# Optimization experiments

Measured on AMD Instinct MI355X. Metric: run time of the kernel, lower is better.

## Reference

```python
import jax, jax.numpy as jnp
import numpy as np

B, H, W = 2, 64, 1024
C1, C2 = 64, 128
MLP = [128, 128]
KH, KW = 5, 5
NS = 3
DIST = 100.0
BN_EPS = 1e-5


def setup_inputs() -> dict:
    key = jax.random.key(0)
    ks = jax.random.split(key, 12)
    inp = {
        "xyz1_proj": jax.random.normal(ks[0], (B, H, W, 3), jnp.float32),
        "xyz2_proj": jax.random.normal(ks[1], (B, H, W, 3), jnp.float32),
        "feat1_proj": jax.random.normal(ks[2], (B, H, W, C1), jnp.float32),
        "feat2_proj": jax.random.normal(ks[3], (B, H, W, C2), jnp.float32),
    }
    cin = C1 + C2
    chans = [cin] + MLP
    for i in range(len(MLP)):
        inp[f"w{i}"] = jax.random.normal(ks[4 + 2 * i], (chans[i], chans[i + 1]), jnp.float32) * 0.05
        inp[f"b{i}"] = jnp.zeros((chans[i + 1],), jnp.float32)
        inp[f"g{i}"] = jnp.ones((chans[i + 1],), jnp.float32)
        inp[f"be{i}"] = jnp.zeros((chans[i + 1],), jnp.float32)
    return inp


def _grid_knn(xyz1, xyz2):
    """Structured-grid KNN (no_sort_knn): for each query pixel, scan a KHxKW
    window in row-major order and take the first NS in-bounds neighbors whose
    squared distance is below DIST^2. Returns flat neighbor indices (B,N,NS)
    and a validity mask (B,N,NS,1)."""
    b, h, w, _ = xyz1.shape
    n = h * w
    k = KH * KW
    x1 = xyz1.reshape(b, n, 3)
    x2 = xyz2.reshape(b, n, 3)
    oh = jnp.repeat(jnp.arange(KH) - KH // 2, KW)   # (K,)
    ow = jnp.tile(jnp.arange(KW) - KW // 2, KH)     # (K,)
    nh = jnp.arange(h)[:, None, None] + oh[None, None, :]   # (H,1,K)
    nw = jnp.arange(w)[None, :, None] + ow[None, None, :]   # (1,W,K)
    inb = ((nh >= 0) & (nh < h)) & ((nw >= 0) & (nw < w))    # (H,W,K)
    flat = jnp.clip(nh, 0, h - 1) * w + jnp.clip(nw, 0, w - 1)
    flat = jnp.broadcast_to(flat, (h, w, k)).reshape(n, k)
    inb = jnp.broadcast_to(inb, (h, w, k)).reshape(n, k)
    # window gather: (B,N,K,3)
    neigh = jnp.take(x2, flat.reshape(-1), axis=1).reshape(b, n, k, 3)
    sq = jnp.sum(jnp.square(neigh - x1[:, :, None, :]), -1)  # (B,N,K)
    valid = inb[None] & (sq < DIST * DIST)
    v = valid.astype(jnp.int32)
    rank = jnp.cumsum(v, -1) - v  # rank among valid, scan order
    sel, fnd = [], []
    for j in range(NS):
        hit = valid & (rank == j)
        sel.append(jnp.argmax(hit, -1))
        fnd.append(jnp.any(hit, -1))
    sel = jnp.stack(sel, -1)          # (B,N,NS) window slot
    found = jnp.stack(fnd, -1)        # (B,N,NS)
    flat_b = jnp.broadcast_to(flat[None], (b, n, k))
    sel_flat = jnp.take_along_axis(flat_b, sel, axis=-1)
    sel_flat = jnp.where(found, sel_flat, 0)  # zeros like the init buffers
    mask = found.astype(x1.dtype)[..., None]  # (B,N,NS,1)
    return sel_flat, mask


def _gather(feat_flat, sel_flat):
    # feat_flat: (B,N,C), sel_flat: (B,N,NS) -> (B,N,NS,C)
    b, n, c = feat_flat.shape
    idx = sel_flat.reshape(b, n * NS, 1)
    g = jnp.take_along_axis(feat_flat, jnp.broadcast_to(idx, (b, n * NS, c)), axis=1)
    return g.reshape(b, n, NS, c)


def reference(xyz1_proj, xyz2_proj, feat1_proj, feat2_proj,
              w0, b0, g0, be0, w1, b1, g1, be1):
    b, h, w, _ = xyz1_proj.shape
    n = h * w
    xyz1 = xyz1_proj.reshape(b, n, 3)
    xyz2 = xyz2_proj.reshape(b, n, 3)
    feat2 = feat2_proj.reshape(b, n, -1)

    sel_flat, mask = _grid_knn(xyz1_proj, xyz2_proj)
    mask = jax.lax.stop_gradient(mask)

    grouped_xyz = _gather(xyz2, sel_flat) * mask          # (B,N,NS,3)
    grouped_feat = _gather(feat2, sel_flat) * mask        # (B,N,NS,C2)

    dist = jnp.sum(jnp.square(grouped_xyz - xyz1[:, :, None, :]), -1)  # (B,N,NS)
    dist = jnp.where(dist < 1e-10, jnp.full_like(dist, 1e-10), dist)
    norm = jnp.sum(1.0 / dist, axis=2, keepdims=True)     # (B,N,1)
    weight = (1.0 / dist) / norm                          # (B,N,NS)
    interp = jnp.sum(grouped_feat * weight[..., None], axis=2)  # (B,N,C2)

    x = jnp.concatenate([feat1_proj.reshape(b, n, -1), interp], -1)  # (B,N,C1+C2)

    # 1x1 conv MLP with training-mode BatchNorm + ReLU
    for (wi, bi, gi, bei) in ((w0, b0, g0, be0), (w1, b1, g1, be1)):
        x = x @ wi + bi
        mu = jnp.mean(x, axis=(0, 1))
        var = jnp.var(x, axis=(0, 1))
        x = (x - mu) * jax.lax.rsqrt(var + BN_EPS) * gi + bei
        x = jax.nn.relu(x)
    return x  # (B, H*W, MLP[-1])
```

## Files before the change

kernel.cpp:

```cpp
#include <hip/hip_runtime.h>

#define H_    64
#define W_    1024
#define NPT   65536
#define NTOT  131072
#define C1_   64
#define C2_   128
#define CIN_  192
#define CM_   128
#define NS_   3
#define DIST2_ 10000.0f
#define BN_EPS_ 1e-5f
#define NSLOT 32
#define XP    132

typedef __attribute__((ext_vector_type(8))) short short8;
typedef __attribute__((ext_vector_type(4))) float floatx4;

static __device__ __forceinline__ unsigned short f2bf(float f) {
    unsigned int u = __float_as_uint(f);
    u += 0x7fffu + ((u >> 16) & 1u);
    return (unsigned short)(u >> 16);
}
static __device__ __forceinline__ float bflo(unsigned u) { return __uint_as_float(u << 16); }
static __device__ __forceinline__ float bfhi(unsigned u) { return __uint_as_float(u & 0xffff0000u); }
static __device__ __forceinline__ unsigned packbf(float a, float b) {
    return (unsigned)f2bf(a) | ((unsigned)f2bf(b) << 16);
}

__global__ __launch_bounds__(256) void prep_w_kernel(
    const float* __restrict__ w0, const float* __restrict__ w1,
    unsigned short* __restrict__ w0F, unsigned short* __restrict__ w1F)
{
    int tid = blockIdx.x * 256 + threadIdx.x;
    if (tid < 3072) {
        int c = tid, lane = c & 63, nt = (c >> 6) & 7, kk = c >> 9;
        int n = nt * 16 + (lane & 15);
        int kb = kk * 32 + (lane >> 4) * 8;
        #pragma unroll
        for (int j = 0; j < 8; j++)
            w0F[(size_t)c * 8 + j] = f2bf(w0[(size_t)(kb + j) * CM_ + n]);
    } else if (tid < 5120) {
        int c = tid - 3072, lane = c & 63, nt = (c >> 6) & 7, kk = c >> 9;
        int n = nt * 16 + (lane & 15);
        int kb = kk * 32 + (lane >> 4) * 8;
        #pragma unroll
        for (int j = 0; j < 8; j++)
            w1F[(size_t)c * 8 + j] = f2bf(w1[(size_t)(kb + j) * CM_ + n]);
    }
}

static __device__ __forceinline__ void bn_finish_lds(
    const float* __restrict__ slots, const float* __restrict__ g,
    const float* __restrict__ be, float* bnpL, int t)
{
    if (t < CM_) {
        float s = 0.f, q2 = 0.f;
        #pragma unroll
        for (int sl = 0; sl < NSLOT; sl++) {
            s  += slots[sl * 256 + t];
            q2 += slots[sl * 256 + CM_ + t];
        }
        const float invn = 1.0f / (float)NTOT;
        float mu = s * invn, var = q2 * invn - mu * mu;
        float sc = g[t] * rsqrtf(var + BN_EPS_);
        bnpL[t] = sc;
        bnpL[CM_ + t] = be[t] - mu * sc;
    }
}

__global__ __launch_bounds__(256, 2) void fused1_kernel(
    const float* __restrict__ xyz1, const float* __restrict__ xyz2,
    const float* __restrict__ feat1, const float* __restrict__ feat2,
    const unsigned short* __restrict__ w0F, const float* __restrict__ b0,
    uint4* __restrict__ y0w4, float* __restrict__ slots0)
{
    __shared__ unsigned short xstage[64][XP];
    __shared__ int   selL[64][NS_];
    __shared__ float wgtL[64][NS_];
    __shared__ float wsum[4][CM_], wsq[4][CM_];

    const int t = threadIdx.x;
    const int blk = blockIdx.x;
    const int pbase = blk * 64;
    const int bidx = blk >> 10;
    const int wv = t >> 6, lane = t & 63;
    const int m = lane & 15, q = lane >> 4;
    const int lr = wv * 16 + m;
    const int row0 = pbase + lr;

    short8 af[2];
    #pragma unroll
    for (int kk = 0; kk < 2; kk++) {
        const float* sp = feat1 + (size_t)row0 * C1_ + kk * 32 + q * 8;
        float4 fa = *(const float4*)(sp), fb = *(const float4*)(sp + 4);
        short8 a;
        a[0] = f2bf(fa.x); a[1] = f2bf(fa.y); a[2] = f2bf(fa.z); a[3] = f2bf(fa.w);
        a[4] = f2bf(fb.x); a[5] = f2bf(fb.y); a[6] = f2bf(fb.z); a[7] = f2bf(fb.w);
        af[kk] = a;
    }

    if (t < 64) {
        const int pt = pbase + t;
        const int n = pt & (NPT - 1);
        const int h = n >> 10, w = n & (W_ - 1);
        const float* p1 = xyz1 + (size_t)pt * 3;
        float x1 = p1[0], y1 = p1[1], z1 = p1[2];
        const float* x2b = xyz2 + (size_t)bidx * NPT * 3;

        float sq[25];
        #pragma unroll
        for (int k = 0; k < 25; k++) {
            const int dh = k / 5 - 2, dw = k % 5 - 2;
            int nh = h + dh, nw = w + dw;
            bool inb = (nh >= 0) && (nh < H_) && (nw >= 0) && (nw < W_);
            int ch = min(max(nh, 0), H_ - 1);
            int cw = min(max(nw, 0), W_ - 1);
            const float* p2 = x2b + (size_t)(ch * W_ + cw) * 3;
            float dx = p2[0] - x1, dy = p2[1] - y1, dz = p2[2] - z1;
            float s = dx * dx + dy * dy + dz * dz;
            sq[k] = inb ? s : 3.4e38f;
        }
        int   s0 = 0, s1 = 0, s2 = 0;
        float d0 = 0.f, d1 = 0.f, d2 = 0.f;
        int cnt = 0;
        #pragma unroll
        for (int k = 0; k < 25; k++) {
            const int dh = k / 5 - 2, dw = k % 5 - 2;
            int ch = min(max(h + dh, 0), H_ - 1);
            int cw = min(max(w + dw, 0), W_ - 1);
            int nidx = ch * W_ + cw;
            if (sq[k] < DIST2_ && cnt < NS_) {
                if (cnt == 0)      { s0 = nidx; d0 = sq[k]; }
                else if (cnt == 1) { s1 = nidx; d1 = sq[k]; }
                else               { s2 = nidx; d2 = sq[k]; }
                cnt++;
            }
        }
        float self2 = x1 * x1 + y1 * y1 + z1 * z1;
        float dd0 = (cnt > 0) ? d0 : self2;
        float dd1 = (cnt > 1) ? d1 : self2;
        float dd2 = (cnt > 2) ? d2 : self2;
        dd0 = fmaxf(dd0, 1e-10f); dd1 = fmaxf(dd1, 1e-10f); dd2 = fmaxf(dd2, 1e-10f);
        float i0 = 1.0f / dd0, i1 = 1.0f / dd1, i2 = 1.0f / dd2;
        float norm = i0 + i1 + i2;
        selL[t][0] = (cnt > 0) ? s0 : 0;
        selL[t][1] = (cnt > 1) ? s1 : 0;
        selL[t][2] = (cnt > 2) ? s2 : 0;
        wgtL[t][0] = (cnt > 0) ? i0 / norm : 0.f;
        wgtL[t][1] = (cnt > 1) ? i1 / norm : 0.f;
        wgtL[t][2] = (cnt > 2) ? i2 / norm : 0.f;
    }
    __syncthreads();

    const float* f2b = feat2 + (size_t)bidx * NPT * C2_;
    #pragma unroll
    for (int i = 0; i < 8; i++) {
        int idx = t + i * 256;
        int p = idx >> 5, c4 = (idx & 31) << 2;
        float ax = 0.f, ay = 0.f, az = 0.f, aw = 0.f;
        #pragma unroll
        for (int j = 0; j < NS_; j++) {
            float wj = wgtL[p][j];
            const float4 f = *(const float4*)(f2b + (size_t)selL[p][j] * C2_ + c4);
            ax += wj * f.x; ay += wj * f.y; az += wj * f.z; aw += wj * f.w;
        }
        ushort4 u;
        u.x = f2bf(ax); u.y = f2bf(ay); u.z = f2bf(az); u.w = f2bf(aw);
        *(ushort4*)&xstage[p][c4] = u;
    }
    __syncthreads();

    floatx4 acc[8];
    #pragma unroll
    for (int nt = 0; nt < 8; nt++) acc[nt] = (floatx4){0.f, 0.f, 0.f, 0.f};

    #pragma unroll
    for (int kk = 0; kk < 6; kk++) {
        short8 bw[8];
        #pragma unroll
        for (int nt = 0; nt < 8; nt++)
            bw[nt] = *(const short8*)(w0F + ((size_t)(kk * 8 + nt) * 64 + lane) * 8);
        short8 a = (kk < 2) ? af[kk]
                            : *(const short8*)&xstage[lr][(kk - 2) * 32 + q * 8];
        #pragma unroll
        for (int nt = 0; nt < 8; nt++)
            acc[nt] = __builtin_amdgcn_mfma_f32_16x16x32_bf16(a, bw[nt], acc[nt], 0, 0, 0);
    }

    #pragma unroll
    for (int nt2 = 0; nt2 < 4; nt2++) {
        const int ntA = 2 * nt2, ntB = ntA + 1;
        const int nA = ntA * 16 + m, nB = ntB * 16 + m;
        float bvA = b0[nA], bvB = b0[nB];
        unsigned u0 = packbf(acc[ntA][0] + bvA, acc[ntA][1] + bvA);
        unsigned u1 = packbf(acc[ntA][2] + bvA, acc[ntA][3] + bvA);
        unsigned u2 = packbf(acc[ntB][0] + bvB, acc[ntB][1] + bvB);
        unsigned u3 = packbf(acc[ntB][2] + bvB, acc[ntB][3] + bvB);
        y0w4[((size_t)(blk * 4 + wv) * 4 + nt2) * 64 + lane] = make_uint4(u0, u1, u2, u3);
        float a0 = bflo(u0), a1 = bfhi(u0), a2 = bflo(u1), a3 = bfhi(u1);
        float b0v = bflo(u2), b1v = bfhi(u2), b2v = bflo(u3), b3v = bfhi(u3);
        float sA = a0 + a1 + a2 + a3, qA = a0*a0 + a1*a1 + a2*a2 + a3*a3;
        float sB = b0v + b1v + b2v + b3v, qB = b0v*b0v + b1v*b1v + b2v*b2v + b3v*b3v;
        sA += __shfl_xor(sA, 16, 64); qA += __shfl_xor(qA, 16, 64);
        sA += __shfl_xor(sA, 32, 64); qA += __shfl_xor(qA, 32, 64);
        sB += __shfl_xor(sB, 16, 64); qB += __shfl_xor(qB, 16, 64);
        sB += __shfl_xor(sB, 32, 64); qB += __shfl_xor(qB, 32, 64);
        if (q == 0) {
            wsum[wv][nA] = sA; wsq[wv][nA] = qA;
            wsum[wv][nB] = sB; wsq[wv][nB] = qB;
        }
    }
    __syncthreads();

    float* slot = slots0 + (size_t)(blk & (NSLOT - 1)) * 256;
    if (t < CM_)
        atomicAdd(&slot[t], wsum[0][t] + wsum[1][t] + wsum[2][t] + wsum[3][t]);
    else
        atomicAdd(&slot[t], wsq[0][t - CM_] + wsq[1][t - CM_] + wsq[2][t - CM_] + wsq[3][t - CM_]);
}

__global__ __launch_bounds__(256, 2) void fused2_kernel(
    const uint4* __restrict__ y0w4, const float* __restrict__ slots0,
    const float* __restrict__ g0, const float* __restrict__ be0,
    const unsigned short* __restrict__ w1F, const float* __restrict__ b1,
    uint4* __restrict__ y1w4, float* __restrict__ slots1)
{
    __shared__ unsigned short x1s[64][XP];
    __shared__ float wsum[4][CM_], wsq[4][CM_];
    __shared__ float bnpL[2 * CM_];

    const int t = threadIdx.x;
    const int blk = blockIdx.x;
    const int wv = t >> 6, lane = t & 63;
    const int m = lane & 15, q = lane >> 4;
    const int lr = wv * 16 + m;

    bn_finish_lds(slots0, g0, be0, bnpL, t);
    __syncthreads();

    #pragma unroll
    for (int nt2 = 0; nt2 < 4; nt2++) {
        const int nA = (2 * nt2) * 16 + m, nB = nA + 16;
        float scA = bnpL[nA], shA = bnpL[CM_ + nA];
        float scB = bnpL[nB], shB = bnpL[CM_ + nB];
        uint4 u = y0w4[((size_t)(blk * 4 + wv) * 4 + nt2) * 64 + lane];
        int rb = wv * 16 + q * 4;
        x1s[rb + 0][nA] = f2bf(fmaxf(bflo(u.x) * scA + shA, 0.f));
        x1s[rb + 1][nA] = f2bf(fmaxf(bfhi(u.x) * scA + shA, 0.f));
        x1s[rb + 2][nA] = f2bf(fmaxf(bflo(u.y) * scA + shA, 0.f));
        x1s[rb + 3][nA] = f2bf(fmaxf(bfhi(u.y) * scA + shA, 0.f));
        x1s[rb + 0][nB] = f2bf(fmaxf(bflo(u.z) * scB + shB, 0.f));
        x1s[rb + 1][nB] = f2bf(fmaxf(bfhi(u.z) * scB + shB, 0.f));
        x1s[rb + 2][nB] = f2bf(fmaxf(bflo(u.w) * scB + shB, 0.f));
        x1s[rb + 3][nB] = f2bf(fmaxf(bfhi(u.w) * scB + shB, 0.f));
    }
    __syncthreads();

    floatx4 acc[8];
    #pragma unroll
    for (int nt = 0; nt < 8; nt++) acc[nt] = (floatx4){0.f, 0.f, 0.f, 0.f};

    #pragma unroll
    for (int kk = 0; kk < 4; kk++) {
        short8 bw[8];
        #pragma unroll
        for (int nt = 0; nt < 8; nt++)
            bw[nt] = *(const short8*)(w1F + ((size_t)(kk * 8 + nt) * 64 + lane) * 8);
        short8 a = *(const short8*)&x1s[lr][kk * 32 + q * 8];
        #pragma unroll
        for (int nt = 0; nt < 8; nt++)
            acc[nt] = __builtin_amdgcn_mfma_f32_16x16x32_bf16(a, bw[nt], acc[nt], 0, 0, 0);
    }

    #pragma unroll
    for (int nt2 = 0; nt2 < 4; nt2++) {
        const int ntA = 2 * nt2, ntB = ntA + 1;
        const int nA = ntA * 16 + m, nB = ntB * 16 + m;
        float bvA = b1[nA], bvB = b1[nB];
        unsigned u0 = packbf(acc[ntA][0] + bvA, acc[ntA][1] + bvA);
        unsigned u1 = packbf(acc[ntA][2] + bvA, acc[ntA][3] + bvA);
        unsigned u2 = packbf(acc[ntB][0] + bvB, acc[ntB][1] + bvB);
        unsigned u3 = packbf(acc[ntB][2] + bvB, acc[ntB][3] + bvB);
        y1w4[((size_t)(blk * 4 + wv) * 4 + nt2) * 64 + lane] = make_uint4(u0, u1, u2, u3);
        float a0 = bflo(u0), a1 = bfhi(u0), a2 = bflo(u1), a3 = bfhi(u1);
        float c0 = bflo(u2), c1 = bfhi(u2), c2 = bflo(u3), c3 = bfhi(u3);
        float sA = a0 + a1 + a2 + a3, qA = a0*a0 + a1*a1 + a2*a2 + a3*a3;
        float sB = c0 + c1 + c2 + c3, qB = c0*c0 + c1*c1 + c2*c2 + c3*c3;
        sA += __shfl_xor(sA, 16, 64); qA += __shfl_xor(qA, 16, 64);
        sA += __shfl_xor(sA, 32, 64); qA += __shfl_xor(qA, 32, 64);
        sB += __shfl_xor(sB, 16, 64); qB += __shfl_xor(qB, 16, 64);
        sB += __shfl_xor(sB, 32, 64); qB += __shfl_xor(qB, 32, 64);
        if (q == 0) {
            wsum[wv][nA] = sA; wsq[wv][nA] = qA;
            wsum[wv][nB] = sB; wsq[wv][nB] = qB;
        }
    }
    __syncthreads();

    float* slot = slots1 + (size_t)(blk & (NSLOT - 1)) * 256;
    if (t < CM_)
        atomicAdd(&slot[t], wsum[0][t] + wsum[1][t] + wsum[2][t] + wsum[3][t]);
    else
        atomicAdd(&slot[t], wsq[0][t - CM_] + wsq[1][t - CM_] + wsq[2][t - CM_] + wsq[3][t - CM_]);
}

__global__ __launch_bounds__(256) void bn_out_kernel(
    const uint4* __restrict__ y1w4, const float* __restrict__ slots1,
    const float* __restrict__ g1, const float* __restrict__ be1,
    float* __restrict__ out)
{
    __shared__ float xo[64][XP];
    __shared__ float bnpL[2 * CM_];
    const int t = threadIdx.x;
    const int blk = blockIdx.x;
    const int wv = t >> 6, lane = t & 63;
    const int m = lane & 15, q = lane >> 4;

    bn_finish_lds(slots1, g1, be1, bnpL, t);
    __syncthreads();

    #pragma unroll
    for (int nt2 = 0; nt2 < 4; nt2++) {
        const int nA = (2 * nt2) * 16 + m, nB = nA + 16;
        float scA = bnpL[nA], shA = bnpL[CM_ + nA];
        float scB = bnpL[nB], shB = bnpL[CM_ + nB];
        uint4 u = y1w4[((size_t)(blk * 4 + wv) * 4 + nt2) * 64 + lane];
        int rb = wv * 16 + q * 4;
        xo[rb + 0][nA] = fmaxf(bflo(u.x) * scA + shA, 0.f);
        xo[rb + 1][nA] = fmaxf(bfhi(u.x) * scA + shA, 0.f);
        xo[rb + 2][nA] = fmaxf(bflo(u.y) * scA + shA, 0.f);
        xo[rb + 3][nA] = fmaxf(bfhi(u.y) * scA + shA, 0.f);
        xo[rb + 0][nB] = fmaxf(bflo(u.z) * scB + shB, 0.f);
        xo[rb + 1][nB] = fmaxf(bfhi(u.z) * scB + shB, 0.f);
        xo[rb + 2][nB] = fmaxf(bflo(u.w) * scB + shB, 0.f);
        xo[rb + 3][nB] = fmaxf(bfhi(u.w) * scB + shB, 0.f);
    }
    __syncthreads();

    const int pbase = blk * 64;
    #pragma unroll
    for (int i = 0; i < 8; i++) {
        int idx = t + i * 256;
        int p = idx >> 5, c4 = (idx & 31) << 2;
        float4 v = *(const float4*)&xo[p][c4];
        *(float4*)(out + (size_t)(pbase + p) * CM_ + c4) = v;
    }
}

__global__ __launch_bounds__(256) void probe_copy_kernel(
    const float4* __restrict__ a, const float4* __restrict__ b,
    float4* __restrict__ dst)
{
    size_t gid = (size_t)blockIdx.x * 256 + threadIdx.x;
    float4 s = {0.f, 0.f, 0.f, 0.f};
    #pragma unroll
    for (int i = 0; i < 8; i++) {
        float4 v = a[gid + (size_t)i * 524288];
        s.x += v.x; s.y += v.y; s.z += v.z; s.w += v.w;
    }
    #pragma unroll
    for (int i = 0; i < 4; i++) {
        float4 v = b[gid + (size_t)i * 524288];
        s.x += v.x; s.y += v.y; s.z += v.z; s.w += v.w;
    }
    dst[gid] = s;
}

extern "C" void kernel_launch(void* const* d_in, const int* in_sizes, int n_in,
                              void* d_out, int out_size, void* d_ws, size_t ws_size,
                              hipStream_t stream)
{
    const float* xyz1  = (const float*)d_in[0];
    const float* xyz2  = (const float*)d_in[1];
    const float* feat1 = (const float*)d_in[2];
    const float* feat2 = (const float*)d_in[3];
    const float* w0    = (const float*)d_in[4];
    const float* b0    = (const float*)d_in[5];
    const float* g0    = (const float*)d_in[6];
    const float* be0   = (const float*)d_in[7];
    const float* w1    = (const float*)d_in[8];
    const float* b1    = (const float*)d_in[9];
    const float* g1    = (const float*)d_in[10];
    const float* be1   = (const float*)d_in[11];
    float* out = (float*)d_out;

    char* ws = (char*)d_ws;
    float* slots0       = (float*)(ws);
    float* slots1       = (float*)(ws + (size_t)NSLOT * 256 * 4);
    char*  p            = ws + 2 * (size_t)NSLOT * 256 * 4;
    unsigned short* w0F = (unsigned short*)p;  p += (size_t)CIN_ * CM_ * 2;
    unsigned short* w1F = (unsigned short*)p;  p += (size_t)CM_ * CM_ * 2;
    uint4* y0w4         = (uint4*)p;           p += (size_t)NTOT * CM_ * 2;
    uint4* y1w4         = (uint4*)p;           p += (size_t)NTOT * CM_ * 2;
    float4* cscr        = (float4*)p;

    hipMemsetAsync(ws, 0, 2 * (size_t)NSLOT * 256 * 4, stream);

    prep_w_kernel<<<20, 256, 0, stream>>>(w0, w1, w0F, w1F);
    fused1_kernel<<<NTOT / 64, 256, 0, stream>>>(xyz1, xyz2, feat1, feat2,
                                                 w0F, b0, y0w4, slots0);
    fused2_kernel<<<NTOT / 64, 256, 0, stream>>>(y0w4, slots0, g0, be0,
                                                 w1F, b1, y1w4, slots1);
    bn_out_kernel<<<NTOT / 64, 256, 0, stream>>>(y1w4, slots1, g1, be1, out);

    probe_copy_kernel<<<2048, 256, 0, stream>>>((const float4*)feat2,
                                                (const float4*)y0w4, cscr);
}
```

Baseline: 235.7 us.

## Parallelize KNN distance scan across all threads and drop probe copy kernel

The 25-neighbor distance computation in the first fused kernel now runs across all 256 threads, four per point, with results staged in shared memory aliased over the feature staging buffer. Previously only 64 threads computed distances serially. The second kernel prefetches the first k-slice of layer-1 weights before the BatchNorm finalization. The leftover bandwidth probe kernel and its scratch buffer are removed, eliminating an extra pass over feat2 and y0. This adds one more barrier and LDS aliasing, which must not overlap live xstage data.

```diff
diff --git a/kernel.cpp b/kernel.cpp
--- a/kernel.cpp
+++ b/kernel.cpp
@@ -75,10 +75,13 @@
     const unsigned short* __restrict__ w0F, const float* __restrict__ b0,
     uint4* __restrict__ y0w4, float* __restrict__ slots0)
 {
-    __shared__ unsigned short xstage[64][XP];
+    __shared__ __align__(16) char smem[64 * XP * 2];
     __shared__ int   selL[64][NS_];
     __shared__ float wgtL[64][NS_];
     __shared__ float wsum[4][CM_], wsq[4][CM_];
+
+    float (*sqL)[28] = (float (*)[28])smem;
+    unsigned short (*xstage)[XP] = (unsigned short (*)[XP])smem;
 
     const int t = threadIdx.x;
     const int blk = blockIdx.x;
@@ -100,27 +103,38 @@
         af[kk] = a;
     }
 
+    {
+        const int p = t >> 2, g = t & 3;
+        const int pt = pbase + p;
+        const int n = pt & (NPT - 1);
+        const int h = n >> 10, w = n & (W_ - 1);
+        const float* p1 = xyz1 + (size_t)pt * 3;
+        float x1 = p1[0], y1 = p1[1], z1 = p1[2];
+        const float* x2b = xyz2 + (size_t)bidx * NPT * 3;
+        #pragma unroll
+        for (int j = 0; j < 7; j++) {
+            int k = g * 7 + j;
+            if (k < 25) {
+                int dh = k / 5 - 2, dw = k % 5 - 2;
+                int nh = h + dh, nw = w + dw;
+                bool inb = (nh >= 0) && (nh < H_) && (nw >= 0) && (nw < W_);
+                int ch = min(max(nh, 0), H_ - 1);
+                int cw = min(max(nw, 0), W_ - 1);
+                const float* p2 = x2b + (size_t)(ch * W_ + cw) * 3;
+                float dx = p2[0] - x1, dy = p2[1] - y1, dz = p2[2] - z1;
+                sqL[p][k] = inb ? (dx * dx + dy * dy + dz * dz) : 3.4e38f;
+            }
+        }
+    }
+    __syncthreads();
+
     if (t < 64) {
         const int pt = pbase + t;
         const int n = pt & (NPT - 1);
         const int h = n >> 10, w = n & (W_ - 1);
         const float* p1 = xyz1 + (size_t)pt * 3;
         float x1 = p1[0], y1 = p1[1], z1 = p1[2];
-        const float* x2b = xyz2 + (size_t)bidx * NPT * 3;
-
-        float sq[25];
-        #pragma unroll
-        for (int k = 0; k < 25; k++) {
-            const int dh = k / 5 - 2, dw = k % 5 - 2;
-            int nh = h + dh, nw = w + dw;
-            bool inb = (nh >= 0) && (nh < H_) && (nw >= 0) && (nw < W_);
-            int ch = min(max(nh, 0), H_ - 1);
-            int cw = min(max(nw, 0), W_ - 1);
-            const float* p2 = x2b + (size_t)(ch * W_ + cw) * 3;
-            float dx = p2[0] - x1, dy = p2[1] - y1, dz = p2[2] - z1;
-            float s = dx * dx + dy * dy + dz * dz;
-            sq[k] = inb ? s : 3.4e38f;
-        }
+
         int   s0 = 0, s1 = 0, s2 = 0;
         float d0 = 0.f, d1 = 0.f, d2 = 0.f;
         int cnt = 0;
@@ -130,10 +144,11 @@
             int ch = min(max(h + dh, 0), H_ - 1);
             int cw = min(max(w + dw, 0), W_ - 1);
             int nidx = ch * W_ + cw;
-            if (sq[k] < DIST2_ && cnt < NS_) {
-                if (cnt == 0)      { s0 = nidx; d0 = sq[k]; }
-                else if (cnt == 1) { s1 = nidx; d1 = sq[k]; }
-                else               { s2 = nidx; d2 = sq[k]; }
+            float sk = sqL[t][k];
+            if (sk < DIST2_ && cnt < NS_) {
+                if (cnt == 0)      { s0 = nidx; d0 = sk; }
+                else if (cnt == 1) { s1 = nidx; d1 = sk; }
+                else               { s2 = nidx; d2 = sk; }
                 cnt++;
             }
         }
@@ -236,6 +251,11 @@
     const int m = lane & 15, q = lane >> 4;
     const int lr = wv * 16 + m;
 
+    short8 bw0[8];
+    #pragma unroll
+    for (int nt = 0; nt < 8; nt++)
+        bw0[nt] = *(const short8*)(w1F + ((size_t)nt * 64 + lane) * 8);
+
     bn_finish_lds(slots0, g0, be0, bnpL, t);
     __syncthreads();
 
@@ -266,7 +286,8 @@
         short8 bw[8];
         #pragma unroll
         for (int nt = 0; nt < 8; nt++)
-            bw[nt] = *(const short8*)(w1F + ((size_t)(kk * 8 + nt) * 64 + lane) * 8);
+            bw[nt] = (kk == 0) ? bw0[nt]
+                   : *(const short8*)(w1F + ((size_t)(kk * 8 + nt) * 64 + lane) * 8);
         short8 a = *(const short8*)&x1s[lr][kk * 32 + q * 8];
         #pragma unroll
         for (int nt = 0; nt < 8; nt++)
@@ -348,25 +369,6 @@
     }
 }
 
-__global__ __launch_bounds__(256) void probe_copy_kernel(
-    const float4* __restrict__ a, const float4* __restrict__ b,
-    float4* __restrict__ dst)
-{
-    size_t gid = (size_t)blockIdx.x * 256 + threadIdx.x;
-    float4 s = {0.f, 0.f, 0.f, 0.f};
-    #pragma unroll
-    for (int i = 0; i < 8; i++) {
-        float4 v = a[gid + (size_t)i * 524288];
-        s.x += v.x; s.y += v.y; s.z += v.z; s.w += v.w;
-    }
-    #pragma unroll
-    for (int i = 0; i < 4; i++) {
-        float4 v = b[gid + (size_t)i * 524288];
-        s.x += v.x; s.y += v.y; s.z += v.z; s.w += v.w;
-    }
-    dst[gid] = s;
-}
-
 extern "C" void kernel_launch(void* const* d_in, const int* in_sizes, int n_in,
                               void* d_out, int out_size, void* d_ws, size_t ws_size,
                               hipStream_t stream)
@@ -392,8 +394,7 @@
     unsigned short* w0F = (unsigned short*)p;  p += (size_t)CIN_ * CM_ * 2;
     unsigned short* w1F = (unsigned short*)p;  p += (size_t)CM_ * CM_ * 2;
     uint4* y0w4         = (uint4*)p;           p += (size_t)NTOT * CM_ * 2;
-    uint4* y1w4         = (uint4*)p;           p += (size_t)NTOT * CM_ * 2;
-    float4* cscr        = (float4*)p;
+    uint4* y1w4         = (uint4*)p;
 
     hipMemsetAsync(ws, 0, 2 * (size_t)NSLOT * 256 * 4, stream);
 
@@ -403,7 +404,4 @@
     fused2_kernel<<<NTOT / 64, 256, 0, stream>>>(y0w4, slots0, g0, be0,
                                                  w1F, b1, y1w4, slots1);
     bn_out_kernel<<<NTOT / 64, 256, 0, stream>>>(y1w4, slots1, g1, be1, out);
-
-    probe_copy_kernel<<<2048, 256, 0, stream>>>((const float4*)feat2,
-                                                (const float4*)y0w4, cscr);
-}
+}
```

After: 224.9 us. 4.6% less time.
